# Performance work log

Hardware: AMD Instinct MI355X
Metric: run time of the kernel (lower is better)

The kernel has to match this reference:

```python
import jax, jax.numpy as jnp
import numpy as np

HEADS, DIM_HEAD, INNER, DIM = 6, 50, 300, 768
HW, EXTRA, POOL = 100, 150, 10  # spatial side, extra tokens, pool output side
N = HW * HW + EXTRA  # 10150


def setup_inputs() -> dict:
    key = jax.random.key(0)
    ks = jax.random.split(key, 6)
    B = 8
    x = jax.random.normal(ks[0], (B, N, DIM), dtype=jnp.float32)
    # weights scaled ~ typical init so softmax logits are sane
    proj_w = jax.random.normal(ks[1], (INNER, DIM), dtype=jnp.float32) * 0.02
    step_x = jax.random.normal(ks[2], (HEADS, 1, 1), dtype=jnp.float32)
    step_rep = jax.random.normal(ks[3], (HEADS, 1, 1), dtype=jnp.float32)
    out_w = jax.random.normal(ks[4], (DIM, INNER), dtype=jnp.float32) * 0.02
    out_b = jax.random.normal(ks[5], (DIM,), dtype=jnp.float32) * 0.02
    return {"x": x, "proj_w": proj_w, "step_x": step_x, "step_rep": step_rep,
            "out_w": out_w, "out_b": out_b}


def reference(x, proj_w, step_x, step_rep, out_w, out_b):
    b, n, c = x.shape
    hw = int(round((n - EXTRA) ** 0.5))
    scale = DIM_HEAD ** -0.5

    w = x @ proj_w.T  # [b, n, 300]

    # adaptive avg pool of the spatial tokens to (10,10); hw % 10 == 0 -> uniform pooling
    k = hw // POOL
    spatial = w[:, : hw * hw, :].reshape(b, hw, hw, INNER).transpose(0, 3, 1, 2)  # [b,300,hw,hw]
    rep = spatial.reshape(b, INNER, POOL, k, POOL, k).mean(axis=(3, 5))  # [b,300,10,10]
    rep = rep.reshape(b, INNER, POOL * POOL).transpose(0, 2, 1)  # [b,100,300]

    wh = w.reshape(b, n, HEADS, DIM_HEAD).transpose(0, 2, 1, 3)        # [b,h,n,d]
    reph = rep.reshape(b, POOL * POOL, HEADS, DIM_HEAD).transpose(0, 2, 1, 3)  # [b,h,100,d]

    # stage 1: rep attends to all tokens
    dots = jnp.einsum('bhqd,bhkd->bhqk', reph, wh) * scale  # [b,h,100,n]
    attn = jax.nn.softmax(dots, axis=-1)
    rep_delta = jnp.einsum('bhqk,bhkd->bhqd', attn, wh)     # [b,h,100,d]
    reph = reph + step_rep * rep_delta

    # stage 2: rep self-attention, broadcast back through reused attn^T
    dots2 = jnp.einsum('bhqd,bhkd->bhqk', reph, reph) * scale  # [b,h,100,100]
    attn2 = jax.nn.softmax(dots2, axis=-1)
    x_delta = jnp.einsum('bhqk,bhkd->bhqd', attn2, reph)       # [b,h,100,d]
    x_delta = jnp.einsum('bhqn,bhqd->bhnd', attn, x_delta)     # attn^T @ x_delta -> [b,h,n,d]
    x_delta = step_x * x_delta

    x_delta = x_delta.transpose(0, 2, 1, 3).reshape(b, n, HEADS * DIM_HEAD)  # [b,n,300]
    return x_delta @ out_w.T + out_b
```

## Files before the change

### kernel.cpp

```cpp
#include <hip/hip_runtime.h>
#include <math.h>

#define BATCH   8
#define NTOK    10150
#define DIMC    768
#define INNERC  300
#define HEADS   6
#define DHEAD   50
#define NQ      100
#define NBH     48
#define NSPLIT  32
#define CHUNK   320
#define SCALE   0.14142135623730951f
#define MTOT    (BATCH*NTOK)
#define XDK     320
#define NEGBIG  -1.0e30f

typedef __attribute__((ext_vector_type(8))) short short8;
typedef __attribute__((ext_vector_type(4))) float f32x4;

__device__ __forceinline__ ushort f2bf(float x) {
  uint u = __float_as_uint(x);
  uint r = (u + 0x7fffu + ((u >> 16) & 1u)) >> 16;
  return (ushort)r;
}
__device__ __forceinline__ float bf2f(ushort h) {
  return __uint_as_float(((uint)h) << 16);
}

__global__ void split_pad(const float* __restrict__ src, ushort* __restrict__ dHi,
                          ushort* __restrict__ dLo, int R, int C, int Rp, int Cp) {
  const int total = Rp * Cp;
  for (int i = blockIdx.x * blockDim.x + threadIdx.x; i < total;
       i += gridDim.x * blockDim.x) {
    const int r = i / Cp, c = i % Cp;
    const float v = (r < R && c < C) ? src[r * C + c] : 0.f;
    const ushort hh = f2bf(v);
    dHi[i] = hh;
    dLo[i] = f2bf(v - bf2f(hh));
  }
}

__global__ void zero_xd_pad(ushort* __restrict__ xdHi, ushort* __restrict__ xdLo) {
  const int total = MTOT * 20;
  for (int i = blockIdx.x * blockDim.x + threadIdx.x; i < total;
       i += gridDim.x * blockDim.x) {
    const size_t g = (size_t)(i / 20) * XDK + 300 + (i % 20);
    xdHi[g] = 0;
    xdLo[g] = 0;
  }
}

__global__ __launch_bounds__(256, 2) void gemm1_xw(
    const float* __restrict__ x, const ushort* __restrict__ pwHi,
    const ushort* __restrict__ pwLo, ushort* __restrict__ wHi,
    ushort* __restrict__ wLo) {
  __shared__ ushort aH[64][40], aL[64][40];
  __shared__ ushort bH[320][40], bL[320][40];
  const int t = threadIdx.x;
  const int lane = t & 63, wv = t >> 6;
  const int l15 = lane & 15, l4 = lane >> 4;
  const int m0 = blockIdx.x * 64;
  const int arow = t >> 2, aslot = t & 3;

  f32x4 acc[4][5];
#pragma unroll
  for (int i = 0; i < 4; ++i)
#pragma unroll
    for (int j = 0; j < 5; ++j) acc[i][j] = (f32x4){0.f, 0.f, 0.f, 0.f};

  for (int k0 = 0; k0 < DIMC; k0 += 32) {
    __syncthreads();
    {
      float v[8];
      const int m = m0 + arow;
      if (m < MTOT) {
        const float* xp = &x[(size_t)m * DIMC + k0 + aslot * 8];
        const float4 u0 = *(const float4*)xp;
        const float4 u1 = *(const float4*)(xp + 4);
        v[0] = u0.x; v[1] = u0.y; v[2] = u0.z; v[3] = u0.w;
        v[4] = u1.x; v[5] = u1.y; v[6] = u1.z; v[7] = u1.w;
      } else {
#pragma unroll
        for (int j = 0; j < 8; ++j) v[j] = 0.f;
      }
      short8 th, tl;
#pragma unroll
      for (int j = 0; j < 8; ++j) {
        const ushort hh = f2bf(v[j]);
        th[j] = (short)hh;
        tl[j] = (short)f2bf(v[j] - bf2f(hh));
      }
      *(short8*)&aH[arow][aslot * 8] = th;
      *(short8*)&aL[arow][aslot * 8] = tl;
    }
#pragma unroll
    for (int i = 0; i < 5; ++i) {
      const int sid = t + i * 256;
      const int row = sid >> 2, slot = sid & 3;
      const size_t g = (size_t)row * DIMC + k0 + slot * 8;
      *(short8*)&bH[row][slot * 8] = *(const short8*)&pwHi[g];
      *(short8*)&bL[row][slot * 8] = *(const short8*)&pwLo[g];
    }
    __syncthreads();

    short8 ah[4], al[4];
#pragma unroll
    for (int i = 0; i < 4; ++i) {
      ah[i] = *(const short8*)&aH[i * 16 + l15][l4 * 8];
      al[i] = *(const short8*)&aL[i * 16 + l15][l4 * 8];
    }
#pragma unroll
    for (int j = 0; j < 5; ++j) {
      const int brow = wv * 80 + j * 16 + l15;
      const short8 bhf = *(const short8*)&bH[brow][l4 * 8];
      const short8 blf = *(const short8*)&bL[brow][l4 * 8];
#pragma unroll
      for (int i = 0; i < 4; ++i) {
        acc[i][j] = __builtin_amdgcn_mfma_f32_16x16x32_bf16(ah[i], bhf, acc[i][j], 0, 0, 0);
        acc[i][j] = __builtin_amdgcn_mfma_f32_16x16x32_bf16(al[i], bhf, acc[i][j], 0, 0, 0);
        acc[i][j] = __builtin_amdgcn_mfma_f32_16x16x32_bf16(ah[i], blf, acc[i][j], 0, 0, 0);
      }
    }
  }

#pragma unroll
  for (int j = 0; j < 5; ++j) {
    const int col = wv * 80 + j * 16 + l15;
    if (col >= INNERC) continue;
#pragma unroll
    for (int i = 0; i < 4; ++i)
#pragma unroll
      for (int r = 0; r < 4; ++r) {
        const int m = m0 + i * 16 + l4 * 4 + r;
        if (m < MTOT) {
          const float val = acc[i][j][r];
          const ushort hh = f2bf(val);
          const size_t g = (size_t)m * INNERC + col;
          wHi[g] = hh;
          wLo[g] = f2bf(val - bf2f(hh));
        }
      }
  }
}

__global__ __launch_bounds__(256, 2) void gemm2_out(
    const ushort* __restrict__ xdHi, const ushort* __restrict__ xdLo,
    const ushort* __restrict__ owHi, const ushort* __restrict__ owLo,
    const float* __restrict__ out_b, float* __restrict__ out) {
  __shared__ ushort aH[64][40], aL[64][40];
  __shared__ ushort bH[256][40], bL[256][40];
  const int t = threadIdx.x;
  const int lane = t & 63, wv = t >> 6;
  const int l15 = lane & 15, l4 = lane >> 4;
  const int nwg = gridDim.x;
  const int q = nwg >> 3, r = nwg & 7;
  const int xcd = blockIdx.x & 7, idx = blockIdx.x >> 3;
  const int wg = (xcd < r ? xcd * (q + 1) : r * (q + 1) + (xcd - r) * q) + idx;
  const int bn = wg % 3, bm = wg / 3;
  const int m0 = bm * 64, n0 = bn * 256;
  const int arow = t >> 2, aslot = t & 3;

  f32x4 acc[4][4];
#pragma unroll
  for (int i = 0; i < 4; ++i)
#pragma unroll
    for (int j = 0; j < 4; ++j) acc[i][j] = (f32x4){0.f, 0.f, 0.f, 0.f};

  for (int k0 = 0; k0 < XDK; k0 += 32) {
    __syncthreads();
    {
      const int m = m0 + arow;
      if (m < MTOT) {
        const size_t g = (size_t)m * XDK + k0 + aslot * 8;
        *(short8*)&aH[arow][aslot * 8] = *(const short8*)&xdHi[g];
        *(short8*)&aL[arow][aslot * 8] = *(const short8*)&xdLo[g];
      } else {
        const short8 z = {0, 0, 0, 0, 0, 0, 0, 0};
        *(short8*)&aH[arow][aslot * 8] = z;
        *(short8*)&aL[arow][aslot * 8] = z;
      }
    }
#pragma unroll
    for (int i = 0; i < 4; ++i) {
      const int sid = t + i * 256;
      const int row = sid >> 2, slot = sid & 3;
      const size_t g = (size_t)(n0 + row) * XDK + k0 + slot * 8;
      *(short8*)&bH[row][slot * 8] = *(const short8*)&owHi[g];
      *(short8*)&bL[row][slot * 8] = *(const short8*)&owLo[g];
    }
    __syncthreads();

    short8 ah[4], al[4];
#pragma unroll
    for (int i = 0; i < 4; ++i) {
      ah[i] = *(const short8*)&aH[i * 16 + l15][l4 * 8];
      al[i] = *(const short8*)&aL[i * 16 + l15][l4 * 8];
    }
#pragma unroll
    for (int j = 0; j < 4; ++j) {
      const int brow = wv * 64 + j * 16 + l15;
      const short8 bhf = *(const short8*)&bH[brow][l4 * 8];
      const short8 blf = *(const short8*)&bL[brow][l4 * 8];
#pragma unroll
      for (int i = 0; i < 4; ++i) {
        acc[i][j] = __builtin_amdgcn_mfma_f32_16x16x32_bf16(ah[i], bhf, acc[i][j], 0, 0, 0);
        acc[i][j] = __builtin_amdgcn_mfma_f32_16x16x32_bf16(al[i], bhf, acc[i][j], 0, 0, 0);
        acc[i][j] = __builtin_amdgcn_mfma_f32_16x16x32_bf16(ah[i], blf, acc[i][j], 0, 0, 0);
      }
    }
  }

#pragma unroll
  for (int j = 0; j < 4; ++j) {
    const int col = n0 + wv * 64 + j * 16 + l15;
    const float bv = out_b[col];
#pragma unroll
    for (int i = 0; i < 4; ++i)
#pragma unroll
      for (int r = 0; r < 4; ++r) {
        const int m = m0 + i * 16 + l4 * 4 + r;
        if (m < MTOT) out[(size_t)m * DIMC + col] = acc[i][j][r] + bv;
      }
  }
}

__global__ void pool_kernel(const ushort* __restrict__ wHi,
                            const ushort* __restrict__ wLo,
                            float* __restrict__ rep) {
  int q = blockIdx.x, b = blockIdx.y;
  int i = threadIdx.x;
  if (i >= INNERC) return;
  int pr = q / 10, pc = q % 10;
  float s = 0.f;
  for (int kr = 0; kr < 10; ++kr)
    for (int kc = 0; kc < 10; ++kc) {
      int tok = (pr * 10 + kr) * 100 + (pc * 10 + kc);
      const size_t g = ((size_t)b * NTOK + tok) * INNERC + i;
      s += bf2f(wHi[g]) + bf2f(wLo[g]);
    }
  s *= 0.01f;
  int h = i / DHEAD, d = i % DHEAD;
  rep[(((size_t)b * HEADS + h) * NQ + q) * DHEAD + d] = s;
}

__global__ __launch_bounds__(256, 3) void attn1_mfma(
    const ushort* __restrict__ wHi, const ushort* __restrict__ wLo,
    const float* __restrict__ rep,
    float* __restrict__ m_part, float* __restrict__ l_part,
    float* __restrict__ delta_part) {
  const int bh = blockIdx.x, s = blockIdx.y;
  const int b = bh / HEADS, h = bh % HEADS;
  const int t = threadIdx.x;
  const int lane = t & 63, wv = t >> 6;
  const int l15 = lane & 15, l4 = lane >> 4;

  __shared__ ushort Khi[32][72], Klo[32][72];
  __shared__ ushort VThi[64][40], VTlo[64][40];
  __shared__ ushort Phi[128][40], Plo[128][40];

  short8 qhi[2][2], qlo[2][2];
#pragma unroll
  for (int mi = 0; mi < 2; ++mi) {
#pragma unroll
    for (int ks = 0; ks < 2; ++ks) {
      const int qr = 32 * wv + 16 * mi + l15;
      short8 th, tl;
#pragma unroll
      for (int j = 0; j < 8; ++j) {
        const int k = 32 * ks + 8 * l4 + j;
        float v = (qr < NQ && k < DHEAD)
                      ? rep[((size_t)bh * NQ + qr) * DHEAD + k] * SCALE : 0.f;
        ushort hh = f2bf(v);
        th[j] = (short)hh;
        tl[j] = (short)f2bf(v - bf2f(hh));
      }
      qhi[mi][ks] = th; qlo[mi][ks] = tl;
    }
  }

  f32x4 accO[2][4];
  float m_run[2][4], l_run[2][4];
#pragma unroll
  for (int mi = 0; mi < 2; ++mi) {
#pragma unroll
    for (int r = 0; r < 4; ++r) { m_run[mi][r] = NEGBIG; l_run[mi][r] = 0.f; }
#pragma unroll
    for (int di = 0; di < 4; ++di) accO[mi][di] = (f32x4){0.f, 0.f, 0.f, 0.f};
  }

  const int n0 = s * CHUNK;
  const int n1 = min(NTOK, n0 + CHUNK);

  for (int nt = n0; nt < n1; nt += 32) {
    __syncthreads();
#pragma unroll
    for (int i = 0; i < 4; ++i) {
      const int idx = t + i * 256;
      const int tr = idx >> 5;
      const int d = (idx & 31) * 2;
      const bool inb = (nt + tr < n1) && (d < DHEAD);
      uint hv = 0, lv = 0;
      if (inb) {
        const size_t g = ((size_t)b * NTOK + nt + tr) * INNERC + h * DHEAD + d;
        hv = *(const uint*)&wHi[g];
        lv = *(const uint*)&wLo[g];
      }
      *(uint*)&Khi[tr][d] = hv;
      *(uint*)&Klo[tr][d] = lv;
      const int ps = ((((tr >> 3) + (d >> 3)) & 3) << 3) + (tr & 7);
      VThi[d][ps] = (ushort)(hv & 0xffffu);
      VTlo[d][ps] = (ushort)(lv & 0xffffu);
      VThi[d + 1][ps] = (ushort)(hv >> 16);
      VTlo[d + 1][ps] = (ushort)(lv >> 16);
    }
    __syncthreads();

    f32x4 accS[2][2];
#pragma unroll
    for (int mi = 0; mi < 2; ++mi)
#pragma unroll
      for (int ni = 0; ni < 2; ++ni) accS[mi][ni] = (f32x4){0.f, 0.f, 0.f, 0.f};
#pragma unroll
    for (int ks = 0; ks < 2; ++ks) {
      short8 kh[2], kl[2];
#pragma unroll
      for (int ni = 0; ni < 2; ++ni) {
        kh[ni] = *(const short8*)&Khi[16 * ni + l15][32 * ks + 8 * l4];
        kl[ni] = *(const short8*)&Klo[16 * ni + l15][32 * ks + 8 * l4];
      }
#pragma unroll
      for (int mi = 0; mi < 2; ++mi)
#pragma unroll
        for (int ni = 0; ni < 2; ++ni) {
          accS[mi][ni] = __builtin_amdgcn_mfma_f32_16x16x32_bf16(qhi[mi][ks], kh[ni], accS[mi][ni], 0, 0, 0);
          accS[mi][ni] = __builtin_amdgcn_mfma_f32_16x16x32_bf16(qlo[mi][ks], kh[ni], accS[mi][ni], 0, 0, 0);
          accS[mi][ni] = __builtin_amdgcn_mfma_f32_16x16x32_bf16(qhi[mi][ks], kl[ni], accS[mi][ni], 0, 0, 0);
        }
    }

    bool cval[2];
#pragma unroll
    for (int ni = 0; ni < 2; ++ni) cval[ni] = (nt + 16 * ni + l15) < n1;
#pragma unroll
    for (int mi = 0; mi < 2; ++mi) {
#pragma unroll
      for (int ni = 0; ni < 2; ++ni)
        if (!cval[ni]) {
#pragma unroll
          for (int r = 0; r < 4; ++r) accS[mi][ni][r] = NEGBIG;
        }
#pragma unroll
      for (int r = 0; r < 4; ++r) {
        float mx = fmaxf(accS[mi][0][r], accS[mi][1][r]);
        mx = fmaxf(mx, __shfl_xor(mx, 1));
        mx = fmaxf(mx, __shfl_xor(mx, 2));
        mx = fmaxf(mx, __shfl_xor(mx, 4));
        mx = fmaxf(mx, __shfl_xor(mx, 8));
        const float m_new = fmaxf(m_run[mi][r], mx);
        const float sc = __expf(m_run[mi][r] - m_new);
        m_run[mi][r] = m_new;
        l_run[mi][r] *= sc;
#pragma unroll
        for (int di = 0; di < 4; ++di) accO[mi][di][r] *= sc;
        float ps = 0.f;
#pragma unroll
        for (int ni = 0; ni < 2; ++ni) {
          const float p = __expf(accS[mi][ni][r] - m_new);
          accS[mi][ni][r] = p;
          ps += p;
        }
        ps += __shfl_xor(ps, 1);
        ps += __shfl_xor(ps, 2);
        ps += __shfl_xor(ps, 4);
        ps += __shfl_xor(ps, 8);
        l_run[mi][r] += ps;
      }
#pragma unroll
      for (int ni = 0; ni < 2; ++ni)
#pragma unroll
        for (int r = 0; r < 4; ++r) {
          const int row = 32 * wv + 16 * mi + 4 * l4 + r;
          const int col = 16 * ni + l15;
          const float p = accS[mi][ni][r];
          const ushort ph = f2bf(p);
          Phi[row][col] = ph;
          Plo[row][col] = f2bf(p - bf2f(ph));
        }
    }

#pragma unroll
    for (int mi = 0; mi < 2; ++mi) {
      const short8 pah = *(const short8*)&Phi[32 * wv + 16 * mi + l15][8 * l4];
      const short8 pal = *(const short8*)&Plo[32 * wv + 16 * mi + l15][8 * l4];
#pragma unroll
      for (int di = 0; di < 4; ++di) {
        const int vs = (((l4 + 2 * di + (l15 >> 3)) & 3)) << 3;
        const short8 vbh = *(const short8*)&VThi[16 * di + l15][vs];
        const short8 vbl = *(const short8*)&VTlo[16 * di + l15][vs];
        accO[mi][di] = __builtin_amdgcn_mfma_f32_16x16x32_bf16(pah, vbh, accO[mi][di], 0, 0, 0);
        accO[mi][di] = __builtin_amdgcn_mfma_f32_16x16x32_bf16(pal, vbh, accO[mi][di], 0, 0, 0);
        accO[mi][di] = __builtin_amdgcn_mfma_f32_16x16x32_bf16(pah, vbl, accO[mi][di], 0, 0, 0);
      }
    }
  }

  const size_t base = ((size_t)bh * NSPLIT + s) * NQ;
#pragma unroll
  for (int mi = 0; mi < 2; ++mi)
#pragma unroll
    for (int r = 0; r < 4; ++r) {
      const int q = 32 * wv + 16 * mi + 4 * l4 + r;
      if (q < NQ && l15 == 0) {
        m_part[base + q] = m_run[mi][r];
        l_part[base + q] = l_run[mi][r];
      }
#pragma unroll
      for (int di = 0; di < 4; ++di) {
        const int d = 16 * di + l15;
        if (q < NQ && d < DHEAD)
          delta_part[(base + q) * DHEAD + d] = accO[mi][di][r];
      }
    }
}

__global__ __launch_bounds__(256) void attn1_combine(
    const float* __restrict__ rep, const float* __restrict__ m_part,
    const float* __restrict__ l_part, const float* __restrict__ delta_part,
    const float* __restrict__ step_rep,
    float* __restrict__ reph2, float* __restrict__ m_fin, float* __restrict__ l_fin) {
  int bh = blockIdx.x;
  int h = bh % HEADS;
  int t = threadIdx.x;
  __shared__ float Mf[NQ], Lf[NQ];
  if (t < NQ) {
    int q = t;
    float M = -INFINITY;
#pragma unroll
    for (int s2 = 0; s2 < NSPLIT; ++s2)
      M = fmaxf(M, m_part[((size_t)bh * NSPLIT + s2) * NQ + q]);
    float L = 0.f;
#pragma unroll
    for (int s2 = 0; s2 < NSPLIT; ++s2)
      L += l_part[((size_t)bh * NSPLIT + s2) * NQ + q] *
           __expf(m_part[((size_t)bh * NSPLIT + s2) * NQ + q] - M);
    Mf[q] = M; Lf[q] = L;
    m_fin[(size_t)bh * NQ + q] = M;
    l_fin[(size_t)bh * NQ + q] = L;
  }
  __syncthreads();
  float sr = step_rep[h];
  for (int idx = t; idx < NQ * DHEAD; idx += 256) {
    int q = idx / DHEAD, d = idx % DHEAD;
    float sum = 0.f;
#pragma unroll
    for (int s2 = 0; s2 < NSPLIT; ++s2) {
      size_t pb = ((size_t)bh * NSPLIT + s2) * NQ + q;
      sum += __expf(m_part[pb] - Mf[q]) * delta_part[pb * DHEAD + d];
    }
    float rd = sum / Lf[q];
    reph2[(size_t)bh * NQ * DHEAD + idx] =
        rep[(size_t)bh * NQ * DHEAD + idx] + sr * rd;
  }
}

__global__ __launch_bounds__(256) void attn2_kernel(
    const float* __restrict__ reph2, const float* __restrict__ step_x,
    float* __restrict__ xq) {
  int bh = blockIdx.x;
  int h = bh % HEADS;
  int t = threadIdx.x;
  __shared__ float r2[NQ * DHEAD];
  __shared__ float att[NQ * NQ];

  for (int idx = t; idx < NQ * DHEAD; idx += 256)
    r2[idx] = reph2[(size_t)bh * NQ * DHEAD + idx];
  __syncthreads();

  for (int idx = t; idx < NQ * NQ; idx += 256) {
    int qq = idx / NQ, jj = idx % NQ;
    float s = 0.f;
#pragma unroll
    for (int k = 0; k < DHEAD; ++k) s += r2[qq * DHEAD + k] * r2[jj * DHEAD + k];
    att[idx] = s * SCALE;
  }
  __syncthreads();
  if (t < NQ) {
    float M = -INFINITY;
    for (int j = 0; j < NQ; ++j) M = fmaxf(M, att[t * NQ + j]);
    float L = 0.f;
    for (int j = 0; j < NQ; ++j) { float e = __expf(att[t * NQ + j] - M); att[t * NQ + j] = e; L += e; }
    float inv = 1.f / L;
    for (int j = 0; j < NQ; ++j) att[t * NQ + j] *= inv;
  }
  __syncthreads();
  float sx = step_x[h];
  for (int idx = t; idx < NQ * DHEAD; idx += 256) {
    int qd_q = idx / DHEAD, d = idx % DHEAD;
    float v = 0.f;
#pragma unroll
    for (int j = 0; j < NQ; ++j) v += att[qd_q * NQ + j] * r2[j * DHEAD + d];
    xq[(size_t)bh * NQ * DHEAD + idx] = sx * v;
  }
}

#define TT3 64
__global__ __launch_bounds__(256, 2) void bcast3_kernel(
    const ushort* __restrict__ wHi, const ushort* __restrict__ wLo,
    const float* __restrict__ rep, const float* __restrict__ xq,
    const float* __restrict__ m_fin, const float* __restrict__ l_fin,
    ushort* __restrict__ xdHi, ushort* __restrict__ xdLo) {
  const int tile = blockIdx.x, bh = blockIdx.y;
  const int b = bh / HEADS, h = bh % HEADS;
  const int tok0 = tile * TT3;
  const int t = threadIdx.x;
  const int lane = t & 63, wv = t >> 6;
  const int l15 = lane & 15, l4 = lane >> 4;

  __shared__ ushort wH[64][72], wL[64][72];
  __shared__ ushort rH[64][72], rL[64][72];
  __shared__ ushort xH[64][72], xL[64][72];
  __shared__ ushort pH[64][72], pL[64][72];

#pragma unroll
  for (int i = 0; i < 8; ++i) {
    const int idx = t + i * 256;
    const int row = idx >> 5;
    const int d = (idx & 31) * 2;
    const int tok = tok0 + row;
    uint hv = 0, lv = 0;
    if (tok < NTOK && d < DHEAD) {
      const size_t g = ((size_t)b * NTOK + tok) * INNERC + h * DHEAD + d;
      hv = *(const uint*)&wHi[g];
      lv = *(const uint*)&wLo[g];
    }
    *(uint*)&wH[row][d] = hv;
    *(uint*)&wL[row][d] = lv;
  }

  f32x4 accO[4];
#pragma unroll
  for (int di = 0; di < 4; ++di) accO[di] = (f32x4){0.f, 0.f, 0.f, 0.f};

  for (int qc = 0; qc < 2; ++qc) {
    const int q0 = qc * 64;
    __syncthreads();
#pragma unroll
    for (int i = 0; i < 4; ++i) {
      const int idx = t + i * 256;
      const int row = idx >> 4;
      const int d0 = (idx & 15) * 4;
      const int q = q0 + row;
      float4 v = make_float4(0.f, 0.f, 0.f, 0.f);
      if (q < NQ && d0 < DHEAD) {
        const float* rp = &rep[((size_t)bh * NQ + q) * DHEAD];
        if (d0 + 3 < DHEAD) v = *(const float4*)&rp[d0];
        else { v.x = rp[d0]; if (d0 + 1 < DHEAD) v.y = rp[d0 + 1]; }
        v.x *= SCALE; v.y *= SCALE; v.z *= SCALE; v.w *= SCALE;
      }
      ushort h0 = f2bf(v.x), h1 = f2bf(v.y), h2 = f2bf(v.z), h3 = f2bf(v.w);
      *(ushort4*)&rH[row][d0] = make_ushort4(h0, h1, h2, h3);
      *(ushort4*)&rL[row][d0] = make_ushort4(f2bf(v.x - bf2f(h0)), f2bf(v.y - bf2f(h1)),
                                             f2bf(v.z - bf2f(h2)), f2bf(v.w - bf2f(h3)));
    }
#pragma unroll
    for (int i = 0; i < 4; ++i) {
      const int idx = t + i * 256;
      const int drow = idx >> 4;
      const int ql0 = (idx & 15) * 4;
      float vv[4] = {0.f, 0.f, 0.f, 0.f};
      if (drow < DHEAD) {
#pragma unroll
        for (int j = 0; j < 4; ++j) {
          const int q = q0 + ql0 + j;
          if (q < NQ) vv[j] = xq[((size_t)bh * NQ + q) * DHEAD + drow];
        }
      }
      ushort h0 = f2bf(vv[0]), h1 = f2bf(vv[1]), h2 = f2bf(vv[2]), h3 = f2bf(vv[3]);
      *(ushort4*)&xH[drow][ql0] = make_ushort4(h0, h1, h2, h3);
      *(ushort4*)&xL[drow][ql0] = make_ushort4(f2bf(vv[0] - bf2f(h0)), f2bf(vv[1] - bf2f(h1)),
                                               f2bf(vv[2] - bf2f(h2)), f2bf(vv[3] - bf2f(h3)));
    }
    __syncthreads();

    f32x4 accS[4];
#pragma unroll
    for (int ni = 0; ni < 4; ++ni) accS[ni] = (f32x4){0.f, 0.f, 0.f, 0.f};
#pragma unroll
    for (int ks = 0; ks < 2; ++ks) {
      const short8 ah = *(const short8*)&wH[wv * 16 + l15][ks * 32 + 8 * l4];
      const short8 al = *(const short8*)&wL[wv * 16 + l15][ks * 32 + 8 * l4];
#pragma unroll
      for (int ni = 0; ni < 4; ++ni) {
        const short8 bhf = *(const short8*)&rH[ni * 16 + l15][ks * 32 + 8 * l4];
        const short8 blf = *(const short8*)&rL[ni * 16 + l15][ks * 32 + 8 * l4];
        accS[ni] = __builtin_amdgcn_mfma_f32_16x16x32_bf16(ah, bhf, accS[ni], 0, 0, 0);
        accS[ni] = __builtin_amdgcn_mfma_f32_16x16x32_bf16(al, bhf, accS[ni], 0, 0, 0);
        accS[ni] = __builtin_amdgcn_mfma_f32_16x16x32_bf16(ah, blf, accS[ni], 0, 0, 0);
      }
    }

#pragma unroll
    for (int ni = 0; ni < 4; ++ni) {
      const int q = q0 + ni * 16 + l15;
      const bool valid = (q < NQ);
      float mq = 0.f, li = 0.f;
      if (valid) {
        mq = m_fin[(size_t)bh * NQ + q];
        li = 1.f / l_fin[(size_t)bh * NQ + q];
      }
#pragma unroll
      for (int r = 0; r < 4; ++r) {
        const float p = valid ? __expf(accS[ni][r] - mq) * li : 0.f;
        const int row = wv * 16 + 4 * l4 + r;
        const ushort ph = f2bf(p);
        pH[row][ni * 16 + l15] = ph;
        pL[row][ni * 16 + l15] = f2bf(p - bf2f(ph));
      }
    }

#pragma unroll
    for (int ks2 = 0; ks2 < 2; ++ks2) {
      const short8 pah = *(const short8*)&pH[wv * 16 + l15][ks2 * 32 + 8 * l4];
      const short8 pal = *(const short8*)&pL[wv * 16 + l15][ks2 * 32 + 8 * l4];
#pragma unroll
      for (int di = 0; di < 4; ++di) {
        const short8 vh = *(const short8*)&xH[di * 16 + l15][ks2 * 32 + 8 * l4];
        const short8 vl = *(const short8*)&xL[di * 16 + l15][ks2 * 32 + 8 * l4];
        accO[di] = __builtin_amdgcn_mfma_f32_16x16x32_bf16(pah, vh, accO[di], 0, 0, 0);
        accO[di] = __builtin_amdgcn_mfma_f32_16x16x32_bf16(pal, vh, accO[di], 0, 0, 0);
        accO[di] = __builtin_amdgcn_mfma_f32_16x16x32_bf16(pah, vl, accO[di], 0, 0, 0);
      }
    }
  }

#pragma unroll
  for (int di = 0; di < 4; ++di) {
    const int d = di * 16 + l15;
    if (d >= DHEAD) continue;
#pragma unroll
    for (int r = 0; r < 4; ++r) {
      const int tok = tok0 + wv * 16 + 4 * l4 + r;
      if (tok < NTOK) {
        const float val = accO[di][r];
        const ushort hh = f2bf(val);
        const size_t g = ((size_t)b * NTOK + tok) * XDK + h * DHEAD + d;
        xdHi[g] = hh;
        xdLo[g] = f2bf(val - bf2f(hh));
      }
    }
  }
}

extern "C" void kernel_launch(void* const* d_in, const int* in_sizes, int n_in,
                              void* d_out, int out_size, void* d_ws, size_t ws_size,
                              hipStream_t stream) {
  const float* x        = (const float*)d_in[0];
  const float* proj_w   = (const float*)d_in[1];
  const float* step_x   = (const float*)d_in[2];
  const float* step_rep = (const float*)d_in[3];
  const float* out_w    = (const float*)d_in[4];
  const float* out_b    = (const float*)d_in[5];
  float* out = (float*)d_out;

  uint8_t* p8 = (uint8_t*)d_ws;
  ushort* wHi    = (ushort*)(p8);
  ushort* wLo    = (ushort*)(p8 + 48720000);
  float*  rep    = (float*) (p8 + 97440000);
  float*  reph2  = (float*) (p8 + 98400000);
  float*  xq     = (float*) (p8 + 99360000);
  float*  m_part = (float*) (p8 + 100320000);
  float*  l_part = (float*) (p8 + 100934400);
  float*  m_fin  = (float*) (p8 + 101548800);
  float*  l_fin  = (float*) (p8 + 101568000);
  ushort* xdHi   = (ushort*)(p8 + 101587200);
  ushort* xdLo   = (ushort*)(p8 + 153555200);
  ushort* pwHi   = (ushort*)(p8 + 205523200);
  ushort* pwLo   = (ushort*)(p8 + 206014720);
  ushort* owHi   = (ushort*)(p8 + 206506240);
  ushort* owLo   = (ushort*)(p8 + 206997760);
  float* delta = (float*)xdHi;

  split_pad<<<960, 256, 0, stream>>>(proj_w, pwHi, pwLo, INNERC, DIMC, 320, DIMC);
  split_pad<<<960, 256, 0, stream>>>(out_w, owHi, owLo, DIMC, INNERC, DIMC, XDK);
  gemm1_xw<<<1269, 256, 0, stream>>>(x, pwHi, pwLo, wHi, wLo);
  pool_kernel<<<dim3(NQ, BATCH), 320, 0, stream>>>(wHi, wLo, rep);
  attn1_mfma<<<dim3(NBH, NSPLIT), 256, 0, stream>>>(wHi, wLo, rep, m_part, l_part, delta);
  attn1_combine<<<NBH, 256, 0, stream>>>(rep, m_part, l_part, delta, step_rep,
                                         reph2, m_fin, l_fin);
  zero_xd_pad<<<2048, 256, 0, stream>>>(xdHi, xdLo);
  attn2_kernel<<<NBH, 256, 0, stream>>>(reph2, step_x, xq);
  bcast3_kernel<<<dim3(159, NBH), 256, 0, stream>>>(wHi, wLo, rep, xq, m_fin, l_fin,
                                                    xdHi, xdLo);
  gemm2_out<<<3807, 256, 0, stream>>>(xdHi, xdLo, owHi, owLo, out_b, out);
}
```

Baseline: 855.6 us.

## Precompute bf16 hi/lo MFMA operand layouts and drop LDS staging in broadcast kernel

The pool and attn2 kernels now also write the scaled rep and the transposed xq as padded bf16 hi/lo split arrays, laid out to match MFMA operands. The broadcast kernel reads these fragments and its w tile straight from global memory into registers, which removes its shared-memory staging, per-block bf16 splitting and most __syncthreads. The smaller LDS footprint allows raising launch bounds to 4 blocks per CU. The cost is redundant, less coalesced global or L2 reads of the rep and xq fragments by every tile.

```diff
diff --git a/kernel.cpp b/kernel.cpp
--- a/kernel.cpp
+++ b/kernel.cpp
@@ -227,21 +227,34 @@
 
 __global__ void pool_kernel(const ushort* __restrict__ wHi,
                             const ushort* __restrict__ wLo,
-                            float* __restrict__ rep) {
+                            float* __restrict__ rep,
+                            ushort* __restrict__ repPH, ushort* __restrict__ repPL) {
   int q = blockIdx.x, b = blockIdx.y;
   int i = threadIdx.x;
-  if (i >= INNERC) return;
-  int pr = q / 10, pc = q % 10;
-  float s = 0.f;
-  for (int kr = 0; kr < 10; ++kr)
-    for (int kc = 0; kc < 10; ++kc) {
-      int tok = (pr * 10 + kr) * 100 + (pc * 10 + kc);
-      const size_t g = ((size_t)b * NTOK + tok) * INNERC + i;
-      s += bf2f(wHi[g]) + bf2f(wLo[g]);
-    }
-  s *= 0.01f;
-  int h = i / DHEAD, d = i % DHEAD;
-  rep[(((size_t)b * HEADS + h) * NQ + q) * DHEAD + d] = s;
+  if (i < INNERC) {
+    int pr = q / 10, pc = q % 10;
+    float s = 0.f;
+    for (int kr = 0; kr < 10; ++kr)
+      for (int kc = 0; kc < 10; ++kc) {
+        int tok = (pr * 10 + kr) * 100 + (pc * 10 + kc);
+        const size_t g = ((size_t)b * NTOK + tok) * INNERC + i;
+        s += bf2f(wHi[g]) + bf2f(wLo[g]);
+      }
+    s *= 0.01f;
+    int h = i / DHEAD, d = i % DHEAD;
+    rep[(((size_t)b * HEADS + h) * NQ + q) * DHEAD + d] = s;
+    const float sv = s * SCALE;
+    const ushort hh = f2bf(sv);
+    const size_t pg = (((size_t)b * HEADS + h) * 128 + q) * 64 + d;
+    repPH[pg] = hh;
+    repPL[pg] = f2bf(sv - bf2f(hh));
+  }
+  for (int j = threadIdx.x; j < HEADS * 14; j += 320) {
+    int h2 = j / 14, d2 = DHEAD + (j % 14);
+    const size_t pg = (((size_t)b * HEADS + h2) * 128 + q) * 64 + d2;
+    repPH[pg] = 0;
+    repPL[pg] = 0;
+  }
 }
 
 __global__ __launch_bounds__(256, 3) void attn1_mfma(
@@ -466,7 +479,7 @@
 
 __global__ __launch_bounds__(256) void attn2_kernel(
     const float* __restrict__ reph2, const float* __restrict__ step_x,
-    float* __restrict__ xq) {
+    ushort* __restrict__ xqTH, ushort* __restrict__ xqTL) {
   int bh = blockIdx.x;
   int h = bh % HEADS;
   int t = threadIdx.x;
@@ -500,14 +513,25 @@
     float v = 0.f;
 #pragma unroll
     for (int j = 0; j < NQ; ++j) v += att[qd_q * NQ + j] * r2[j * DHEAD + d];
-    xq[(size_t)bh * NQ * DHEAD + idx] = sx * v;
+    v *= sx;
+    const size_t pg = ((size_t)bh * 64 + d) * 128 + qd_q;
+    const ushort hh = f2bf(v);
+    xqTH[pg] = hh;
+    xqTL[pg] = f2bf(v - bf2f(hh));
+  }
+  for (int idx = t; idx < 64 * 28; idx += 256) {
+    int d = idx / 28, qq2 = NQ + (idx % 28);
+    const size_t pg = ((size_t)bh * 64 + d) * 128 + qq2;
+    xqTH[pg] = 0;
+    xqTL[pg] = 0;
   }
 }
 
 #define TT3 64
-__global__ __launch_bounds__(256, 2) void bcast3_kernel(
+__global__ __launch_bounds__(256, 4) void bcast4_kernel(
     const ushort* __restrict__ wHi, const ushort* __restrict__ wLo,
-    const float* __restrict__ rep, const float* __restrict__ xq,
+    const ushort* __restrict__ repPH, const ushort* __restrict__ repPL,
+    const ushort* __restrict__ xqTH, const ushort* __restrict__ xqTL,
     const float* __restrict__ m_fin, const float* __restrict__ l_fin,
     ushort* __restrict__ xdHi, ushort* __restrict__ xdLo) {
   const int tile = blockIdx.x, bh = blockIdx.y;
@@ -517,92 +541,62 @@
   const int lane = t & 63, wv = t >> 6;
   const int l15 = lane & 15, l4 = lane >> 4;
 
-  __shared__ ushort wH[64][72], wL[64][72];
-  __shared__ ushort rH[64][72], rL[64][72];
-  __shared__ ushort xH[64][72], xL[64][72];
   __shared__ ushort pH[64][72], pL[64][72];
 
-#pragma unroll
-  for (int i = 0; i < 8; ++i) {
-    const int idx = t + i * 256;
-    const int row = idx >> 5;
-    const int d = (idx & 31) * 2;
-    const int tok = tok0 + row;
-    uint hv = 0, lv = 0;
-    if (tok < NTOK && d < DHEAD) {
-      const size_t g = ((size_t)b * NTOK + tok) * INNERC + h * DHEAD + d;
-      hv = *(const uint*)&wHi[g];
-      lv = *(const uint*)&wLo[g];
-    }
-    *(uint*)&wH[row][d] = hv;
-    *(uint*)&wL[row][d] = lv;
+  const int tokA = tok0 + 16 * wv + l15;
+  short8 awh[2], awl[2];
+#pragma unroll
+  for (int ks = 0; ks < 2; ++ks) {
+    const int kbase = 32 * ks + 8 * l4;
+    uint hv[4] = {0, 0, 0, 0}, lv[4] = {0, 0, 0, 0};
+    if (tokA < NTOK && kbase < DHEAD) {
+      const size_t g = ((size_t)b * NTOK + tokA) * INNERC + h * DHEAD + kbase;
+#pragma unroll
+      for (int c = 0; c < 4; ++c) {
+        hv[c] = *(const uint*)&wHi[g + 2 * c];
+        lv[c] = *(const uint*)&wLo[g + 2 * c];
+      }
+    }
+    short8 th, tl;
+#pragma unroll
+    for (int j = 0; j < 8; ++j) {
+      const bool ok = (kbase + j) < DHEAD;
+      const ushort hsel = (j & 1) ? (ushort)(hv[j >> 1] >> 16) : (ushort)(hv[j >> 1] & 0xffffu);
+      const ushort lsel = (j & 1) ? (ushort)(lv[j >> 1] >> 16) : (ushort)(lv[j >> 1] & 0xffffu);
+      th[j] = ok ? (short)hsel : (short)0;
+      tl[j] = ok ? (short)lsel : (short)0;
+    }
+    awh[ks] = th;
+    awl[ks] = tl;
   }
 
   f32x4 accO[4];
 #pragma unroll
   for (int di = 0; di < 4; ++di) accO[di] = (f32x4){0.f, 0.f, 0.f, 0.f};
 
+#pragma unroll
   for (int qc = 0; qc < 2; ++qc) {
     const int q0 = qc * 64;
-    __syncthreads();
-#pragma unroll
-    for (int i = 0; i < 4; ++i) {
-      const int idx = t + i * 256;
-      const int row = idx >> 4;
-      const int d0 = (idx & 15) * 4;
-      const int q = q0 + row;
-      float4 v = make_float4(0.f, 0.f, 0.f, 0.f);
-      if (q < NQ && d0 < DHEAD) {
-        const float* rp = &rep[((size_t)bh * NQ + q) * DHEAD];
-        if (d0 + 3 < DHEAD) v = *(const float4*)&rp[d0];
-        else { v.x = rp[d0]; if (d0 + 1 < DHEAD) v.y = rp[d0 + 1]; }
-        v.x *= SCALE; v.y *= SCALE; v.z *= SCALE; v.w *= SCALE;
-      }
-      ushort h0 = f2bf(v.x), h1 = f2bf(v.y), h2 = f2bf(v.z), h3 = f2bf(v.w);
-      *(ushort4*)&rH[row][d0] = make_ushort4(h0, h1, h2, h3);
-      *(ushort4*)&rL[row][d0] = make_ushort4(f2bf(v.x - bf2f(h0)), f2bf(v.y - bf2f(h1)),
-                                             f2bf(v.z - bf2f(h2)), f2bf(v.w - bf2f(h3)));
-    }
-#pragma unroll
-    for (int i = 0; i < 4; ++i) {
-      const int idx = t + i * 256;
-      const int drow = idx >> 4;
-      const int ql0 = (idx & 15) * 4;
-      float vv[4] = {0.f, 0.f, 0.f, 0.f};
-      if (drow < DHEAD) {
-#pragma unroll
-        for (int j = 0; j < 4; ++j) {
-          const int q = q0 + ql0 + j;
-          if (q < NQ) vv[j] = xq[((size_t)bh * NQ + q) * DHEAD + drow];
-        }
-      }
-      ushort h0 = f2bf(vv[0]), h1 = f2bf(vv[1]), h2 = f2bf(vv[2]), h3 = f2bf(vv[3]);
-      *(ushort4*)&xH[drow][ql0] = make_ushort4(h0, h1, h2, h3);
-      *(ushort4*)&xL[drow][ql0] = make_ushort4(f2bf(vv[0] - bf2f(h0)), f2bf(vv[1] - bf2f(h1)),
-                                               f2bf(vv[2] - bf2f(h2)), f2bf(vv[3] - bf2f(h3)));
-    }
-    __syncthreads();
 
     f32x4 accS[4];
 #pragma unroll
     for (int ni = 0; ni < 4; ++ni) accS[ni] = (f32x4){0.f, 0.f, 0.f, 0.f};
 #pragma unroll
     for (int ks = 0; ks < 2; ++ks) {
-      const short8 ah = *(const short8*)&wH[wv * 16 + l15][ks * 32 + 8 * l4];
-      const short8 al = *(const short8*)&wL[wv * 16 + l15][ks * 32 + 8 * l4];
 #pragma unroll
       for (int ni = 0; ni < 4; ++ni) {
-        const short8 bhf = *(const short8*)&rH[ni * 16 + l15][ks * 32 + 8 * l4];
-        const short8 blf = *(const short8*)&rL[ni * 16 + l15][ks * 32 + 8 * l4];
-        accS[ni] = __builtin_amdgcn_mfma_f32_16x16x32_bf16(ah, bhf, accS[ni], 0, 0, 0);
-        accS[ni] = __builtin_amdgcn_mfma_f32_16x16x32_bf16(al, bhf, accS[ni], 0, 0, 0);
-        accS[ni] = __builtin_amdgcn_mfma_f32_16x16x32_bf16(ah, blf, accS[ni], 0, 0, 0);
+        const size_t rg = (((size_t)bh * 128) + (q0 + 16 * ni + l15)) * 64 + 32 * ks + 8 * l4;
+        const short8 rbh = *(const short8*)&repPH[rg];
+        const short8 rbl = *(const short8*)&repPL[rg];
+        accS[ni] = __builtin_amdgcn_mfma_f32_16x16x32_bf16(awh[ks], rbh, accS[ni], 0, 0, 0);
+        accS[ni] = __builtin_amdgcn_mfma_f32_16x16x32_bf16(awl[ks], rbh, accS[ni], 0, 0, 0);
+        accS[ni] = __builtin_amdgcn_mfma_f32_16x16x32_bf16(awh[ks], rbl, accS[ni], 0, 0, 0);
       }
     }
 
 #pragma unroll
     for (int ni = 0; ni < 4; ++ni) {
-      const int q = q0 + ni * 16 + l15;
+      const int q = q0 + 16 * ni + l15;
       const bool valid = (q < NQ);
       float mq = 0.f, li = 0.f;
       if (valid) {
@@ -612,24 +606,25 @@
 #pragma unroll
       for (int r = 0; r < 4; ++r) {
         const float p = valid ? __expf(accS[ni][r] - mq) * li : 0.f;
-        const int row = wv * 16 + 4 * l4 + r;
+        const int row = 16 * wv + 4 * l4 + r;
         const ushort ph = f2bf(p);
-        pH[row][ni * 16 + l15] = ph;
-        pL[row][ni * 16 + l15] = f2bf(p - bf2f(ph));
+        pH[row][16 * ni + l15] = ph;
+        pL[row][16 * ni + l15] = f2bf(p - bf2f(ph));
       }
     }
 
 #pragma unroll
     for (int ks2 = 0; ks2 < 2; ++ks2) {
-      const short8 pah = *(const short8*)&pH[wv * 16 + l15][ks2 * 32 + 8 * l4];
-      const short8 pal = *(const short8*)&pL[wv * 16 + l15][ks2 * 32 + 8 * l4];
+      const short8 pah = *(const short8*)&pH[16 * wv + l15][32 * ks2 + 8 * l4];
+      const short8 pal = *(const short8*)&pL[16 * wv + l15][32 * ks2 + 8 * l4];
 #pragma unroll
       for (int di = 0; di < 4; ++di) {
-        const short8 vh = *(const short8*)&xH[di * 16 + l15][ks2 * 32 + 8 * l4];
-        const short8 vl = *(const short8*)&xL[di * 16 + l15][ks2 * 32 + 8 * l4];
-        accO[di] = __builtin_amdgcn_mfma_f32_16x16x32_bf16(pah, vh, accO[di], 0, 0, 0);
-        accO[di] = __builtin_amdgcn_mfma_f32_16x16x32_bf16(pal, vh, accO[di], 0, 0, 0);
-        accO[di] = __builtin_amdgcn_mfma_f32_16x16x32_bf16(pah, vl, accO[di], 0, 0, 0);
+        const size_t xg = (((size_t)bh * 64) + (16 * di + l15)) * 128 + q0 + 32 * ks2 + 8 * l4;
+        const short8 vbh = *(const short8*)&xqTH[xg];
+        const short8 vbl = *(const short8*)&xqTL[xg];
+        accO[di] = __builtin_amdgcn_mfma_f32_16x16x32_bf16(pah, vbh, accO[di], 0, 0, 0);
+        accO[di] = __builtin_amdgcn_mfma_f32_16x16x32_bf16(pal, vbh, accO[di], 0, 0, 0);
+        accO[di] = __builtin_amdgcn_mfma_f32_16x16x32_bf16(pah, vbl, accO[di], 0, 0, 0);
       }
     }
   }
@@ -668,7 +663,6 @@
   ushort* wLo    = (ushort*)(p8 + 48720000);
   float*  rep    = (float*) (p8 + 97440000);
   float*  reph2  = (float*) (p8 + 98400000);
-  float*  xq     = (float*) (p8 + 99360000);
   float*  m_part = (float*) (p8 + 100320000);
   float*  l_part = (float*) (p8 + 100934400);
   float*  m_fin  = (float*) (p8 + 101548800);
@@ -679,18 +673,22 @@
   ushort* pwLo   = (ushort*)(p8 + 206014720);
   ushort* owHi   = (ushort*)(p8 + 206506240);
   ushort* owLo   = (ushort*)(p8 + 206997760);
+  ushort* repPH  = (ushort*)(p8 + 207489280);
+  ushort* repPL  = (ushort*)(p8 + 208275712);
+  ushort* xqTH   = (ushort*)(p8 + 209062144);
+  ushort* xqTL   = (ushort*)(p8 + 209848576);
   float* delta = (float*)xdHi;
 
   split_pad<<<960, 256, 0, stream>>>(proj_w, pwHi, pwLo, INNERC, DIMC, 320, DIMC);
   split_pad<<<960, 256, 0, stream>>>(out_w, owHi, owLo, DIMC, INNERC, DIMC, XDK);
   gemm1_xw<<<1269, 256, 0, stream>>>(x, pwHi, pwLo, wHi, wLo);
-  pool_kernel<<<dim3(NQ, BATCH), 320, 0, stream>>>(wHi, wLo, rep);
+  pool_kernel<<<dim3(NQ, BATCH), 320, 0, stream>>>(wHi, wLo, rep, repPH, repPL);
   attn1_mfma<<<dim3(NBH, NSPLIT), 256, 0, stream>>>(wHi, wLo, rep, m_part, l_part, delta);
   attn1_combine<<<NBH, 256, 0, stream>>>(rep, m_part, l_part, delta, step_rep,
                                          reph2, m_fin, l_fin);
   zero_xd_pad<<<2048, 256, 0, stream>>>(xdHi, xdLo);
-  attn2_kernel<<<NBH, 256, 0, stream>>>(reph2, step_x, xq);
-  bcast3_kernel<<<dim3(159, NBH), 256, 0, stream>>>(wHi, wLo, rep, xq, m_fin, l_fin,
-                                                    xdHi, xdLo);
+  attn2_kernel<<<NBH, 256, 0, stream>>>(reph2, step_x, xqTH, xqTL);
+  bcast4_kernel<<<dim3(159, NBH), 256, 0, stream>>>(
+      wHi, wLo, repPH, repPL, xqTH, xqTL, m_fin, l_fin, xdHi, xdLo);
   gemm2_out<<<3807, 256, 0, stream>>>(xdHi, xdLo, owHi, owLo, out_b, out);
 }
```

New measurement: 850.2 us. No clear change (-0.6%).
